# Kernel optimization log

Hardware: AMD Instinct MI355X
Metric: run time of the kernel (lower is better)

The kernel has to match this reference:

```python
import jax, jax.numpy as jnp
import numpy as np

INTRA_K = 16
OUTER_K = 16
MAX_PAIR = 1024


def _mahalanobis(x, cov_inv, mean):
    # x: (..., D) difference vectors; returns squared Mahalanobis-style form (...,)
    xc = x - mean
    return jnp.einsum('...i,ij,...j->...', xc, cov_inv, xc)


def setup_inputs() -> dict:
    key = jax.random.key(0)
    k1, k2, k3 = jax.random.split(key, 3)
    B, N, M = 4, 1024, 1024
    outputs = jax.random.normal(k1, (B, N, 9), dtype=jnp.float32)
    targets = jax.random.normal(k2, (B, M, 9), dtype=jnp.float32)
    mask = jax.random.randint(k3, (B, M), 0, 2).astype(bool)
    return {"outputs": outputs, "targets": targets, "mask": mask}


def reference(outputs, targets, mask):
    y_pred = outputs[:, :MAX_PAIR]                      # (B, N, 9)
    m = mask.astype(y_pred.dtype)                       # (B, M)
    cnt = m.sum()

    # mean / covariance over masked true grasps (equivalent to boolean-gather)
    mean = (targets * m[..., None]).sum((0, 1)) / cnt   # (9,)
    centered = (targets - mean) * m[..., None]          # masked rows contribute 0
    flat = centered.reshape(-1, 9)
    cov = flat.T @ flat / (cnt - 1.0)                   # (9, 9)
    cov_inv = jnp.linalg.pinv(cov)

    # intra loss: true-vs-pred pairwise distances, masked rows excluded
    diff = targets[:, :, None, :] - y_pred[:, None, :, :]   # (B, M, N, 9)
    d = _mahalanobis(diff, cov_inv, mean)                   # (B, M, N)
    neg_topk, _ = jax.lax.top_k(-d, INTRA_K)                # k smallest
    row_sum = (-neg_topk).sum(-1)                           # (B, M)
    intra_loss = (row_sum * m).sum() / cnt                  # mean over masked rows

    # outer loss: pred-vs-pred pairwise distances, no mask
    diff_r = y_pred[:, None, :, :] - y_pred[:, :, None, :]  # (B, N, N, 9); [b,i,j] = pred[b,j]-pred[b,i]
    d_r = _mahalanobis(diff_r, cov_inv, mean)               # (B, N, N)
    neg_tk, _ = jax.lax.top_k(-d_r, OUTER_K)
    outer_loss = (-neg_tk).mean()

    return intra_loss, intra_loss, outer_loss
```

## Files before the change

kernel.cpp:

```cpp
#include <hip/hip_runtime.h>
#include <math.h>

#define BB    4
#define MM    1024
#define NN    1024
#define DD    9
#define KSEL  16
#define NROW  (BB * MM)
#define NBLKD (2 * NROW / 4)

struct Ws {
  float yT[BB * DD * NN];
  float qy[BB * NN];
  float bpart[NBLKD];
  float part[16][55];
  float cnt;
  float mean[DD];
  float cinv[DD * DD];
  unsigned ticket;
};

__global__ __launch_bounds__(256) void stats_kernel(
    const float* __restrict__ targets, const int* __restrict__ mask,
    Ws* __restrict__ ws) {
  const int tid = threadIdx.x;
  const int r = blockIdx.x * 256 + tid;
  if (blockIdx.x == 0 && tid == 0) ws->ticket = 0u;

  float acc[55];
#pragma unroll
  for (int k = 0; k < 55; ++k) acc[k] = 0.f;
  if (mask[r] != 0) {
    float t[DD];
#pragma unroll
    for (int k = 0; k < DD; ++k) t[k] = targets[r * DD + k];
    acc[0] = 1.f;
#pragma unroll
    for (int k = 0; k < DD; ++k) acc[1 + k] = t[k];
    int u = 10;
#pragma unroll
    for (int p = 0; p < DD; ++p)
#pragma unroll
      for (int q = p; q < DD; ++q) acc[u++] = t[p] * t[q];
  }

  __shared__ float lds[4][55];
#pragma unroll
  for (int k = 0; k < 55; ++k) {
    float v = acc[k];
#pragma unroll
    for (int off = 32; off > 0; off >>= 1) v += __shfl_down(v, off, 64);
    if ((tid & 63) == 0) lds[tid >> 6][k] = v;
  }
  __syncthreads();
  if (tid < 55)
    ws->part[blockIdx.x][tid] =
        lds[0][tid] + lds[1][tid] + lds[2][tid] + lds[3][tid];
}

__global__ __launch_bounds__(256) void prep_kernel(
    const float* __restrict__ outputs, Ws* __restrict__ ws) {
  const int tid = threadIdx.x;
  __shared__ double Sd[55];
  __shared__ float Cs[DD * DD];

  if (tid < 55) {
    double s = 0.0;
#pragma unroll
    for (int b = 0; b < 16; ++b) s += (double)ws->part[b][tid];
    Sd[tid] = s;
  }
  __syncthreads();

  if (tid < 64) {
    const double cnt = Sd[0];
    const int p = (tid < DD) ? tid : 0;
    double row[2 * DD];
    {
      const double mu_p = Sd[1 + p] / cnt;
#pragma unroll
      for (int q = 0; q < DD; ++q) {
        const int pp = (p < q) ? p : q;
        const int qq = (p < q) ? q : p;
        const int idx = 10 + 9 * pp - (pp * (pp - 1)) / 2 + (qq - pp);
        row[q] = (Sd[idx] - cnt * mu_p * (Sd[1 + q] / cnt)) / (cnt - 1.0);
        row[DD + q] = (p == q) ? 1.0 : 0.0;
      }
    }
#pragma unroll
    for (int c = 0; c < DD; ++c) {
      const double diag = __shfl(row[c], c, 64);
      const double dinv = 1.0 / diag;
      if (tid == c) {
#pragma unroll
        for (int q = 0; q < 2 * DD; ++q) row[q] *= dinv;
      }
      const double f = (tid == c) ? 0.0 : row[c];
#pragma unroll
      for (int q = 0; q < 2 * DD; ++q) {
        const double pv = __shfl(row[q], c, 64);
        row[q] -= f * pv;
      }
    }
    if (tid < DD) {
#pragma unroll
      for (int q = 0; q < DD; ++q) {
        const float cf = (float)row[DD + q];
        Cs[tid * DD + q] = cf;
        if (blockIdx.x == 0) ws->cinv[tid * DD + q] = cf;
      }
    }
    if (tid == 0 && blockIdx.x == 0) {
      ws->cnt = (float)cnt;
#pragma unroll
      for (int q = 0; q < DD; ++q) ws->mean[q] = (float)(Sd[1 + q] / cnt);
    }
  }
  __syncthreads();

  const int j = blockIdx.x * 256 + tid;
  const int b = j >> 10;
  const int jj = j & (NN - 1);
  float y[DD];
#pragma unroll
  for (int k = 0; k < DD; ++k) y[k] = outputs[j * DD + k];
  float q = 0.f;
#pragma unroll
  for (int p = 0; p < DD; ++p) {
    float s = 0.f;
#pragma unroll
    for (int t = 0; t < DD; ++t) s += Cs[p * DD + t] * y[t];
    q += y[p] * s;
    ws->yT[(b * DD + p) * NN + jj] = y[p];
  }
  ws->qy[j] = q;
}

__device__ __forceinline__ float topk16_sum(float v[16]) {
#pragma unroll
  for (int k = 2; k <= 16; k <<= 1) {
#pragma unroll
    for (int j = k >> 1; j > 0; j >>= 1) {
#pragma unroll
      for (int i = 0; i < 16; ++i) {
        const int l = i ^ j;
        if (l > i) {
          const bool up = ((i & k) == 0);
          const float lo = fminf(v[i], v[l]);
          const float hi = fmaxf(v[i], v[l]);
          v[i] = up ? lo : hi;
          v[l] = up ? hi : lo;
        }
      }
    }
  }
#pragma unroll
  for (int off = 1; off < 64; off <<= 1) {
    float pr[16];
#pragma unroll
    for (int i = 0; i < 16; ++i) pr[i] = __shfl_xor(v[i], off, 64);
#pragma unroll
    for (int i = 0; i < 16; ++i) v[i] = fminf(v[i], pr[15 - i]);
    if (off < 32) {
#pragma unroll
      for (int j = 8; j > 0; j >>= 1) {
#pragma unroll
        for (int i = 0; i < 16; ++i) {
          const int l = i ^ j;
          if (l > i) {
            const float lo = fminf(v[i], v[l]);
            const float hi = fmaxf(v[i], v[l]);
            v[i] = lo;
            v[l] = hi;
          }
        }
      }
    }
  }
  float t = v[0];
#pragma unroll
  for (int k = 1; k < 16; ++k) t += v[k];
  return t;
}

__global__ __launch_bounds__(256) void dist_kernel(
    const float* __restrict__ outputs, const float* __restrict__ targets,
    const int* __restrict__ mask, Ws* __restrict__ ws,
    float* __restrict__ out) {
  const int wv = threadIdx.x >> 6;
  const int lane = threadIdx.x & 63;
  const int s = blockIdx.x * 4 + wv;
  const bool is_intra = (s < NROW);
  const int r = s & (NROW - 1);
  const int b = r >> 10;

  float total = 0.f;
  if (!(is_intra && mask[r] == 0)) {
    float a[DD];
    if (is_intra) {
#pragma unroll
      for (int k = 0; k < DD; ++k) a[k] = targets[r * DD + k] - ws->mean[k];
    } else {
#pragma unroll
      for (int k = 0; k < DD; ++k) a[k] = outputs[r * DD + k] + ws->mean[k];
    }
    float w9[DD];
    float qa = 0.f;
#pragma unroll
    for (int p = 0; p < DD; ++p) {
      float acc = 0.f;
#pragma unroll
      for (int t = 0; t < DD; ++t) acc += ws->cinv[p * DD + t] * a[t];
      w9[p] = acc;
      qa += a[p] * acc;
    }

    float v[16];
#pragma unroll
    for (int k = 0; k < 16; ++k) v[k] = 0.f;
    const float* __restrict__ yTb = ws->yT + (size_t)b * DD * NN;
#pragma unroll
    for (int p = 0; p < DD; ++p) {
      const float4* __restrict__ pl = (const float4*)(yTb + (size_t)p * NN);
      const float wp = w9[p];
#pragma unroll
      for (int c = 0; c < 4; ++c) {
        const float4 y4 = pl[c * 64 + lane];
        v[c * 4 + 0] += wp * y4.x;
        v[c * 4 + 1] += wp * y4.y;
        v[c * 4 + 2] += wp * y4.z;
        v[c * 4 + 3] += wp * y4.w;
      }
    }
    {
      const float4* __restrict__ q4 = (const float4*)(ws->qy + (size_t)b * NN);
#pragma unroll
      for (int c = 0; c < 4; ++c) {
        const float4 qv = q4[c * 64 + lane];
        v[c * 4 + 0] = qa + qv.x - 2.f * v[c * 4 + 0];
        v[c * 4 + 1] = qa + qv.y - 2.f * v[c * 4 + 1];
        v[c * 4 + 2] = qa + qv.z - 2.f * v[c * 4 + 2];
        v[c * 4 + 3] = qa + qv.w - 2.f * v[c * 4 + 3];
      }
    }
    total = topk16_sum(v);
  }

  __shared__ float bsum[4];
  __shared__ int s_last;
  if (lane == 0) bsum[wv] = total;
  __syncthreads();
  if (threadIdx.x == 0) {
    const float sblk = bsum[0] + bsum[1] + bsum[2] + bsum[3];
    const float old = atomicExch(&ws->bpart[blockIdx.x], sblk);
    unsigned inc = 1u;
    asm volatile("" : "+v"(inc) : "v"(old));
    const unsigned t = atomicAdd(&ws->ticket, inc);
    s_last = (t == NBLKD - 1) ? 1 : 0;
  }
  __syncthreads();

  if (s_last) {
    double li = 0.0, lo = 0.0;
    for (int k = threadIdx.x; k < NBLKD; k += 256) {
      const double pv = (double)atomicAdd(&ws->bpart[k], 0.f);
      if (k < NBLKD / 2) li += pv; else lo += pv;
    }
#pragma unroll
    for (int off = 32; off > 0; off >>= 1) {
      li += __shfl_down(li, off, 64);
      lo += __shfl_down(lo, off, 64);
    }
    __shared__ double ri[4], ro[4];
    if (lane == 0) { ri[wv] = li; ro[wv] = lo; }
    __syncthreads();
    if (threadIdx.x == 0) {
      const double si = ri[0] + ri[1] + ri[2] + ri[3];
      const double so = ro[0] + ro[1] + ro[2] + ro[3];
      const float intra = (float)(si / (double)ws->cnt);
      const float outer = (float)(so / (double)(NROW * KSEL));
      out[0] = intra;
      out[1] = intra;
      out[2] = outer;
    }
  }
}

extern "C" void kernel_launch(void* const* d_in, const int* in_sizes, int n_in,
                              void* d_out, int out_size, void* d_ws,
                              size_t ws_size, hipStream_t stream) {
  const float* outputs = (const float*)d_in[0];
  const float* targets = (const float*)d_in[1];
  const int* mask = (const int*)d_in[2];
  Ws* ws = (Ws*)d_ws;
  float* out = (float*)d_out;

  stats_kernel<<<NROW / 256, 256, 0, stream>>>(targets, mask, ws);
  prep_kernel<<<(BB * NN) / 256, 256, 0, stream>>>(outputs, ws);
  dist_kernel<<<NBLKD, 256, 0, stream>>>(outputs, targets, mask, ws, out);
}
```

Before: 111.5 us.

## Fold stats into redundant per-block prep and replace atomic ticket with finalize kernel

Each of the 16 prep blocks now recomputes the full masked mean and covariance moments over all 4096 target rows, which removes the separate stats kernel and its cross-block partial buffer. The distance kernel writes per-row top-k sums to a buffer and returns early for masked rows. A new single-block finalize kernel reduces those sums, replacing the atomic ticket and last-block reduction. This trades redundant statistics work in every prep block and one extra launch for fewer atomics and no last-block serialization.

```diff
diff --git a/kernel.cpp b/kernel.cpp
--- a/kernel.cpp
+++ b/kernel.cpp
@@ -7,44 +7,46 @@
 #define DD    9
 #define KSEL  16
 #define NROW  (BB * MM)
-#define NBLKD (2 * NROW / 4)
+#define NSLOT (2 * NROW)
+#define NBLKD (NSLOT / 4)
 
 struct Ws {
   float yT[BB * DD * NN];
   float qy[BB * NN];
-  float bpart[NBLKD];
-  float part[16][55];
+  float rowsum[NSLOT];
   float cnt;
   float mean[DD];
   float cinv[DD * DD];
-  unsigned ticket;
 };
 
-__global__ __launch_bounds__(256) void stats_kernel(
-    const float* __restrict__ targets, const int* __restrict__ mask,
-    Ws* __restrict__ ws) {
+__global__ __launch_bounds__(256) void prep_kernel(
+    const float* __restrict__ outputs, const float* __restrict__ targets,
+    const int* __restrict__ mask, Ws* __restrict__ ws) {
   const int tid = threadIdx.x;
-  const int r = blockIdx.x * 256 + tid;
-  if (blockIdx.x == 0 && tid == 0) ws->ticket = 0u;
+  __shared__ float lds[4][55];
+  __shared__ double Sd[55];
+  __shared__ float Cs[DD * DD];
 
   float acc[55];
 #pragma unroll
   for (int k = 0; k < 55; ++k) acc[k] = 0.f;
-  if (mask[r] != 0) {
-    float t[DD];
-#pragma unroll
-    for (int k = 0; k < DD; ++k) t[k] = targets[r * DD + k];
-    acc[0] = 1.f;
-#pragma unroll
-    for (int k = 0; k < DD; ++k) acc[1 + k] = t[k];
-    int u = 10;
-#pragma unroll
-    for (int p = 0; p < DD; ++p)
-#pragma unroll
-      for (int q = p; q < DD; ++q) acc[u++] = t[p] * t[q];
-  }
-
-  __shared__ float lds[4][55];
+#pragma unroll
+  for (int it = 0; it < NROW / 256; ++it) {
+    const int r = it * 256 + tid;
+    if (mask[r] != 0) {
+      float t[DD];
+#pragma unroll
+      for (int k = 0; k < DD; ++k) t[k] = targets[r * DD + k];
+      acc[0] += 1.f;
+#pragma unroll
+      for (int k = 0; k < DD; ++k) acc[1 + k] += t[k];
+      int u = 10;
+#pragma unroll
+      for (int p = 0; p < DD; ++p)
+#pragma unroll
+        for (int q = p; q < DD; ++q) acc[u++] += t[p] * t[q];
+    }
+  }
 #pragma unroll
   for (int k = 0; k < 55; ++k) {
     float v = acc[k];
@@ -54,22 +56,8 @@
   }
   __syncthreads();
   if (tid < 55)
-    ws->part[blockIdx.x][tid] =
-        lds[0][tid] + lds[1][tid] + lds[2][tid] + lds[3][tid];
-}
-
-__global__ __launch_bounds__(256) void prep_kernel(
-    const float* __restrict__ outputs, Ws* __restrict__ ws) {
-  const int tid = threadIdx.x;
-  __shared__ double Sd[55];
-  __shared__ float Cs[DD * DD];
-
-  if (tid < 55) {
-    double s = 0.0;
-#pragma unroll
-    for (int b = 0; b < 16; ++b) s += (double)ws->part[b][tid];
-    Sd[tid] = s;
-  }
+    Sd[tid] = (double)lds[0][tid] + (double)lds[1][tid] + (double)lds[2][tid] +
+              (double)lds[3][tid];
   __syncthreads();
 
   if (tid < 64) {
@@ -185,8 +173,7 @@
 
 __global__ __launch_bounds__(256) void dist_kernel(
     const float* __restrict__ outputs, const float* __restrict__ targets,
-    const int* __restrict__ mask, Ws* __restrict__ ws,
-    float* __restrict__ out) {
+    const int* __restrict__ mask, Ws* __restrict__ ws) {
   const int wv = threadIdx.x >> 6;
   const int lane = threadIdx.x & 63;
   const int s = blockIdx.x * 4 + wv;
@@ -194,95 +181,90 @@
   const int r = s & (NROW - 1);
   const int b = r >> 10;
 
-  float total = 0.f;
-  if (!(is_intra && mask[r] == 0)) {
-    float a[DD];
-    if (is_intra) {
-#pragma unroll
-      for (int k = 0; k < DD; ++k) a[k] = targets[r * DD + k] - ws->mean[k];
-    } else {
-#pragma unroll
-      for (int k = 0; k < DD; ++k) a[k] = outputs[r * DD + k] + ws->mean[k];
-    }
-    float w9[DD];
-    float qa = 0.f;
-#pragma unroll
-    for (int p = 0; p < DD; ++p) {
-      float acc = 0.f;
-#pragma unroll
-      for (int t = 0; t < DD; ++t) acc += ws->cinv[p * DD + t] * a[t];
-      w9[p] = acc;
-      qa += a[p] * acc;
-    }
-
-    float v[16];
-#pragma unroll
-    for (int k = 0; k < 16; ++k) v[k] = 0.f;
-    const float* __restrict__ yTb = ws->yT + (size_t)b * DD * NN;
-#pragma unroll
-    for (int p = 0; p < DD; ++p) {
-      const float4* __restrict__ pl = (const float4*)(yTb + (size_t)p * NN);
-      const float wp = w9[p];
-#pragma unroll
-      for (int c = 0; c < 4; ++c) {
-        const float4 y4 = pl[c * 64 + lane];
-        v[c * 4 + 0] += wp * y4.x;
-        v[c * 4 + 1] += wp * y4.y;
-        v[c * 4 + 2] += wp * y4.z;
-        v[c * 4 + 3] += wp * y4.w;
-      }
-    }
-    {
-      const float4* __restrict__ q4 = (const float4*)(ws->qy + (size_t)b * NN);
-#pragma unroll
-      for (int c = 0; c < 4; ++c) {
-        const float4 qv = q4[c * 64 + lane];
-        v[c * 4 + 0] = qa + qv.x - 2.f * v[c * 4 + 0];
-        v[c * 4 + 1] = qa + qv.y - 2.f * v[c * 4 + 1];
-        v[c * 4 + 2] = qa + qv.z - 2.f * v[c * 4 + 2];
-        v[c * 4 + 3] = qa + qv.w - 2.f * v[c * 4 + 3];
-      }
-    }
-    total = topk16_sum(v);
-  }
-
-  __shared__ float bsum[4];
-  __shared__ int s_last;
-  if (lane == 0) bsum[wv] = total;
-  __syncthreads();
-  if (threadIdx.x == 0) {
-    const float sblk = bsum[0] + bsum[1] + bsum[2] + bsum[3];
-    const float old = atomicExch(&ws->bpart[blockIdx.x], sblk);
-    unsigned inc = 1u;
-    asm volatile("" : "+v"(inc) : "v"(old));
-    const unsigned t = atomicAdd(&ws->ticket, inc);
-    s_last = (t == NBLKD - 1) ? 1 : 0;
-  }
-  __syncthreads();
-
-  if (s_last) {
-    double li = 0.0, lo = 0.0;
-    for (int k = threadIdx.x; k < NBLKD; k += 256) {
-      const double pv = (double)atomicAdd(&ws->bpart[k], 0.f);
-      if (k < NBLKD / 2) li += pv; else lo += pv;
-    }
-#pragma unroll
-    for (int off = 32; off > 0; off >>= 1) {
-      li += __shfl_down(li, off, 64);
-      lo += __shfl_down(lo, off, 64);
-    }
-    __shared__ double ri[4], ro[4];
-    if (lane == 0) { ri[wv] = li; ro[wv] = lo; }
-    __syncthreads();
-    if (threadIdx.x == 0) {
-      const double si = ri[0] + ri[1] + ri[2] + ri[3];
-      const double so = ro[0] + ro[1] + ro[2] + ro[3];
-      const float intra = (float)(si / (double)ws->cnt);
-      const float outer = (float)(so / (double)(NROW * KSEL));
-      out[0] = intra;
-      out[1] = intra;
-      out[2] = outer;
-    }
+  if (is_intra && mask[r] == 0) {
+    if (lane == 0) ws->rowsum[s] = 0.f;
+    return;
+  }
+
+  float a[DD];
+  if (is_intra) {
+#pragma unroll
+    for (int k = 0; k < DD; ++k) a[k] = targets[r * DD + k] - ws->mean[k];
+  } else {
+#pragma unroll
+    for (int k = 0; k < DD; ++k) a[k] = outputs[r * DD + k] + ws->mean[k];
+  }
+  float w9[DD];
+  float qa = 0.f;
+#pragma unroll
+  for (int p = 0; p < DD; ++p) {
+    float acc = 0.f;
+#pragma unroll
+    for (int t = 0; t < DD; ++t) acc += ws->cinv[p * DD + t] * a[t];
+    w9[p] = acc;
+    qa += a[p] * acc;
+  }
+
+  float v[16];
+#pragma unroll
+  for (int k = 0; k < 16; ++k) v[k] = 0.f;
+  const float* __restrict__ yTb = ws->yT + (size_t)b * DD * NN;
+#pragma unroll
+  for (int p = 0; p < DD; ++p) {
+    const float4* __restrict__ pl = (const float4*)(yTb + (size_t)p * NN);
+    const float wp = w9[p];
+#pragma unroll
+    for (int c = 0; c < 4; ++c) {
+      const float4 y4 = pl[c * 64 + lane];
+      v[c * 4 + 0] += wp * y4.x;
+      v[c * 4 + 1] += wp * y4.y;
+      v[c * 4 + 2] += wp * y4.z;
+      v[c * 4 + 3] += wp * y4.w;
+    }
+  }
+  {
+    const float4* __restrict__ q4 = (const float4*)(ws->qy + (size_t)b * NN);
+#pragma unroll
+    for (int c = 0; c < 4; ++c) {
+      const float4 qv = q4[c * 64 + lane];
+      v[c * 4 + 0] = qa + qv.x - 2.f * v[c * 4 + 0];
+      v[c * 4 + 1] = qa + qv.y - 2.f * v[c * 4 + 1];
+      v[c * 4 + 2] = qa + qv.z - 2.f * v[c * 4 + 2];
+      v[c * 4 + 3] = qa + qv.w - 2.f * v[c * 4 + 3];
+    }
+  }
+
+  const float total = topk16_sum(v);
+  if (lane == 0) ws->rowsum[s] = total;
+}
+
+__global__ __launch_bounds__(256) void finalize_kernel(
+    const Ws* __restrict__ ws, float* __restrict__ out) {
+  const int tid = threadIdx.x;
+  double li = 0.0, lo = 0.0;
+  for (int k = tid; k < NROW; k += 256) {
+    li += (double)ws->rowsum[k];
+    lo += (double)ws->rowsum[NROW + k];
+  }
+#pragma unroll
+  for (int off = 32; off > 0; off >>= 1) {
+    li += __shfl_down(li, off, 64);
+    lo += __shfl_down(lo, off, 64);
+  }
+  __shared__ double lds_i[4], lds_o[4];
+  if ((tid & 63) == 0) {
+    lds_i[tid >> 6] = li;
+    lds_o[tid >> 6] = lo;
+  }
+  __syncthreads();
+  if (tid == 0) {
+    const double si = lds_i[0] + lds_i[1] + lds_i[2] + lds_i[3];
+    const double so = lds_o[0] + lds_o[1] + lds_o[2] + lds_o[3];
+    const float intra = (float)(si / (double)ws->cnt);
+    const float outer = (float)(so / (double)(NROW * KSEL));
+    out[0] = intra;
+    out[1] = intra;
+    out[2] = outer;
   }
 }
 
@@ -295,7 +277,7 @@
   Ws* ws = (Ws*)d_ws;
   float* out = (float*)d_out;
 
-  stats_kernel<<<NROW / 256, 256, 0, stream>>>(targets, mask, ws);
-  prep_kernel<<<(BB * NN) / 256, 256, 0, stream>>>(outputs, ws);
-  dist_kernel<<<NBLKD, 256, 0, stream>>>(outputs, targets, mask, ws, out);
-}
+  prep_kernel<<<16, 256, 0, stream>>>(outputs, targets, mask, ws);
+  dist_kernel<<<NBLKD, 256, 0, stream>>>(outputs, targets, mask, ws);
+  finalize_kernel<<<1, 256, 0, stream>>>(ws, out);
+}
```

New measurement: 105.4 us. 1.06x faster.
